# Kernel tuning notes

Measured on AMD Instinct MI355X. Metric: run time of the kernel, lower is better.

Reference implementation:

```python
import jax, jax.numpy as jnp
import numpy as np

DELTA_COEFF = 1.0
CLAMP_MIN = 1e-3  # hardcoded in original clamp(min=0.001)


def setup_inputs() -> dict:
    key = jax.random.key(0)
    k1, k2, k3 = jax.random.split(key, 3)
    B, N, F_in, F_out = 2, 1024, 128, 64
    x = jax.random.normal(k1, (B, N, F_in), dtype=jnp.float32)
    adj = jax.random.uniform(k2, (B, N, N), dtype=jnp.float32)
    weight = jax.random.normal(k3, (F_in, F_out), dtype=jnp.float32) * (1.0 / np.sqrt(F_in))
    bias = jnp.zeros((F_out,), dtype=jnp.float32)
    return {"x": x, "adj": adj, "weight": weight, "bias": bias}


def reference(x, adj, weight, bias):
    # x: [B,N,F_in], adj: [B,N,N]
    x = x @ weight  # [B,N,F_out]
    B, N, _ = adj.shape
    # pairwise L1 distance: [B,N,N]
    abs_diff = jnp.sum(jnp.abs(x[:, :, None, :] - x[:, None, :, :]), axis=-1)
    mod_adj = adj / jnp.maximum(abs_diff, CLAMP_MIN)
    deg = jnp.sum(mod_adj, axis=-1)  # [B,N]
    # Laplacian L = D - A~ ; then I - delta * L
    lap = jnp.zeros_like(mod_adj).at[:, jnp.arange(N), jnp.arange(N)].set(deg) - mod_adj
    mod = jnp.eye(N, dtype=x.dtype) - DELTA_COEFF * lap
    out = jnp.matmul(mod, x) + bias
    return out
```

## Files before the change

### kernel.cpp

```cpp
#include <hip/hip_runtime.h>
#include <hip/hip_fp16.h>


#define JS 16
#define HSTR 72

typedef _Float16 half8_t __attribute__((ext_vector_type(8)));
typedef float    f32x4_t __attribute__((ext_vector_type(4)));

__global__ __launch_bounds__(256) void gemm_xw(const float* __restrict__ x,
                                               const float* __restrict__ w,
                                               float* __restrict__ xw,
                                               __half* __restrict__ xwh,
                                               __half* __restrict__ xwt) {
    __shared__ float ws_[128 * 64];
    __shared__ float xs[8 * 132];
    __shared__ __half ts[8 * 64];
    const int tid = threadIdx.x;
    const int r0  = blockIdx.x * 8;

#pragma unroll
    for (int e = tid; e < 2048; e += 256)
        ((float4*)ws_)[e] = ((const float4*)w)[e];
    {
        int row = tid >> 5, c = tid & 31;
        float4 v = *(const float4*)&x[(size_t)(r0 + row) * 128 + c * 4];
        *(float4*)&xs[row * 132 + c * 4] = v;
    }
    __syncthreads();

    const int rl = tid >> 5;
    const int fg = tid & 31;
    float2 acc = {0.f, 0.f};
#pragma unroll 8
    for (int k = 0; k < 128; ++k) {
        float xv = xs[rl * 132 + k];
        float2 wv = *(const float2*)&ws_[k * 64 + 2 * fg];
        acc.x += xv * wv.x; acc.y += xv * wv.y;
    }
    size_t o = (size_t)(r0 + rl) * 64 + 2 * fg;
    *(float2*)&xw[o] = acc;
    __half2 h2 = __floats2half2_rn(acc.x, acc.y);
    *(__half2*)&xwh[o] = h2;
    *(__half2*)&ts[rl * 64 + 2 * fg] = h2;
    __syncthreads();

    if (tid < 64) {
        const int f = tid;
        const int b = r0 >> 10;
        const int n0 = r0 & 1023;
        __half hv[8];
#pragma unroll
        for (int r = 0; r < 8; ++r) hv[r] = ts[r * 64 + f];
        *(half8_t*)&xwt[((size_t)(b * 64 + f)) * 1024 + n0] = *(half8_t*)hv;
    }
}

template <bool ATOMIC>
__global__ __launch_bounds__(256) void fused_gtv(const __half* __restrict__ xwh,
                                                 const __half* __restrict__ xwt,
                                                 const float* __restrict__ adj,
                                                 float* __restrict__ pout,
                                                 float* __restrict__ pdeg) {
    __shared__ __half xih[32 * HSTR];
    __shared__ __half xjh[64 * HSTR];
    __shared__ __half xjt[64 * HSTR];
    __shared__ __half wt[32 * HSTR];

    const int tid = threadIdx.x;
    const int bx  = blockIdx.x;
    const int js  = bx & 15;
    const int it  = (bx >> 4) & 31;
    const int b   = bx >> 9;
    const int i0  = it * 32;
    const int j0  = js * 64;

    const __half* xhb = xwh + (size_t)b * 65536;
    const __half* xtb = xwt + (size_t)b * 65536;
    const float*  adjb = adj + (size_t)b * 1048576;

    const int ty = tid >> 5;
    const int tx = tid & 31;

    float2 av[4];
#pragma unroll
    for (int r = 0; r < 4; ++r)
        av[r] = *(const float2*)&adjb[(size_t)(i0 + 4 * ty + r) * 1024 + j0 + 2 * tx];

    {
        int row = tid >> 3, c = tid & 7;
        float4 v = *(const float4*)&xhb[(i0 + row) * 64 + c * 8];
        *(float4*)&xih[row * HSTR + c * 8] = v;
    }
#pragma unroll
    for (int e = tid; e < 512; e += 256) {
        int row = e >> 3, c = e & 7;
        float4 v = *(const float4*)&xhb[(j0 + row) * 64 + c * 8];
        *(float4*)&xjh[row * HSTR + c * 8] = v;
        float4 t = *(const float4*)&xtb[row * 1024 + j0 + c * 8];
        *(float4*)&xjt[row * HSTR + c * 8] = t;
    }
    __syncthreads();

    __half2 acc[4][2];
#pragma unroll
    for (int r = 0; r < 4; ++r)
#pragma unroll
        for (int q = 0; q < 2; ++q) acc[r][q] = __floats2half2_rn(0.f, 0.f);

#pragma unroll
    for (int c = 0; c < 8; ++c) {
        float4 a[4], bb[2];
#pragma unroll
        for (int r = 0; r < 4; ++r)
            a[r] = *(const float4*)&xih[(4 * ty + r) * HSTR + c * 8];
#pragma unroll
        for (int q = 0; q < 2; ++q)
            bb[q] = *(const float4*)&xjh[(2 * tx + q) * HSTR + c * 8];
#pragma unroll
        for (int r = 0; r < 4; ++r) {
            const __half2* pa = (const __half2*)&a[r];
#pragma unroll
            for (int q = 0; q < 2; ++q) {
                const __half2* pb = (const __half2*)&bb[q];
#pragma unroll
                for (int m = 0; m < 4; ++m)
                    acc[r][q] = __hadd2(acc[r][q], __habs2(__hsub2(pa[m], pb[m])));
            }
        }
    }

    float dsum[4];
#pragma unroll
    for (int r = 0; r < 4; ++r) {
        const int gi = i0 + 4 * ty + r;
        float wv[2];
#pragma unroll
        for (int q = 0; q < 2; ++q) {
            const int gj = j0 + 2 * tx + q;
            float d = __low2float(acc[r][q]) + __high2float(acc[r][q]);
            float v = (&av[r].x)[q] / fmaxf(d, 1e-3f);
            wv[q] = (gi == gj) ? 0.f : v;
        }
        *(__half2*)&wt[(4 * ty + r) * HSTR + 2 * tx] = __floats2half2_rn(wv[0], wv[1]);
        dsum[r] = wv[0] + wv[1];
    }
#pragma unroll
    for (int r = 0; r < 4; ++r) {
#pragma unroll
        for (int m = 1; m < 32; m <<= 1)
            dsum[r] += __shfl_xor(dsum[r], m, 32);
    }
    if (tx == 0) {
#pragma unroll
        for (int r = 0; r < 4; ++r) {
            if (ATOMIC) atomicAdd(&pdeg[b * 1024 + i0 + 4 * ty + r], dsum[r]);
            else pdeg[(js * 2 + b) * 1024 + i0 + 4 * ty + r] = dsum[r];
        }
    }
    __syncthreads();

    const int wv   = tid >> 6;
    const int lane = tid & 63;
    const int quad = lane >> 4;
    const int l15  = lane & 15;
    const int m16  = wv & 1;
    const int npair = wv >> 1;

    f32x4_t c0 = {0.f, 0.f, 0.f, 0.f};
    f32x4_t c1 = {0.f, 0.f, 0.f, 0.f};
#pragma unroll
    for (int s = 0; s < 2; ++s) {
        half8_t af = *(half8_t*)&wt[(m16 * 16 + l15) * HSTR + s * 32 + quad * 8];
        half8_t b0 = *(half8_t*)&xjt[((npair * 2 + 0) * 16 + l15) * HSTR + s * 32 + quad * 8];
        half8_t b1 = *(half8_t*)&xjt[((npair * 2 + 1) * 16 + l15) * HSTR + s * 32 + quad * 8];
        c0 = __builtin_amdgcn_mfma_f32_16x16x32_f16(af, b0, c0, 0, 0, 0);
        c1 = __builtin_amdgcn_mfma_f32_16x16x32_f16(af, b1, c1, 0, 0, 0);
    }

    if (ATOMIC) {
#pragma unroll
        for (int r = 0; r < 4; ++r) {
            int row = m16 * 16 + quad * 4 + r;
            atomicAdd(&pout[((size_t)b * 1024 + i0 + row) * 64 + (npair * 2) * 16 + l15], c0[r]);
            atomicAdd(&pout[((size_t)b * 1024 + i0 + row) * 64 + (npair * 2 + 1) * 16 + l15], c1[r]);
        }
    } else {
        const size_t slot = (size_t)(js * 2 + b) * 65536;
#pragma unroll
        for (int r = 0; r < 4; ++r) {
            int row = m16 * 16 + quad * 4 + r;
            pout[slot + (i0 + row) * 64 + (npair * 2) * 16 + l15] = c0[r];
            pout[slot + (i0 + row) * 64 + (npair * 2 + 1) * 16 + l15] = c1[r];
        }
    }
}

template <bool ATOMIC>
__global__ __launch_bounds__(256) void finish_gtv(const float* __restrict__ xw,
                                                  const float* __restrict__ part,
                                                  const float* __restrict__ pdeg,
                                                  const float* __restrict__ bias,
                                                  float* __restrict__ out) {
    int idx = blockIdx.x * 256 + threadIdx.x;
    int f = idx & 63;
    int r = idx >> 6;
    int b = r >> 10;
    if (ATOMIC) {
        out[idx] = out[idx] + (1.f - pdeg[r]) * xw[idx] + bias[f];
    } else {
        int loc = idx & 65535;
        int n   = r & 1023;
        float s = 0.f, dgs = 0.f;
#pragma unroll
        for (int js = 0; js < JS; ++js) {
            s   += part[(size_t)(js * 2 + b) * 65536 + loc];
            dgs += pdeg[(js * 2 + b) * 1024 + n];
        }
        out[idx] = s + (1.f - dgs) * xw[idx] + bias[f];
    }
}

extern "C" void kernel_launch(void* const* d_in, const int* in_sizes, int n_in,
                              void* d_out, int out_size, void* d_ws, size_t ws_size,
                              hipStream_t stream) {
    const float* x    = (const float*)d_in[0];
    const float* adj  = (const float*)d_in[1];
    const float* w    = (const float*)d_in[2];
    const float* bias = (const float*)d_in[3];
    float* out = (float*)d_out;

    char* wsb = (char*)d_ws;
    float*  xw   = (float*)wsb;
    __half* xwh  = (__half*)(wsb + 512 * 1024);
    __half* xwt  = (__half*)(wsb + 768 * 1024);
    float*  pdeg = (float*)(wsb + 1024 * 1024);
    float*  part = (float*)(wsb + 1152 * 1024);
    const size_t NEED = 1152 * 1024 + (size_t)32 * 65536 * 4;

    gemm_xw<<<256, 256, 0, stream>>>(x, w, xw, xwh, xwt);

    if (ws_size >= NEED) {
        fused_gtv<false><<<1024, 256, 0, stream>>>(xwh, xwt, adj, part, pdeg);
        finish_gtv<false><<<512, 256, 0, stream>>>(xw, part, pdeg, bias, out);
    } else {
        hipMemsetAsync(out, 0, 2 * 1024 * 64 * sizeof(float), stream);
        hipMemsetAsync(pdeg, 0, 2 * 1024 * sizeof(float), stream);
        fused_gtv<true><<<1024, 256, 0, stream>>>(xwh, xwt, adj, out, pdeg);
        finish_gtv<true><<<512, 256, 0, stream>>>(xw, nullptr, pdeg, bias, out);
    }
}
```

Before: 85.08 us.

## Enlarge fused tile to 64x64, swizzle LDS, store fp16 partials, vectorize xw GEMM

Each block of the fused kernel now covers a 64x64 i-j tile instead of 32x64, with a 4x4 per-thread micro-tile and four MFMA output tiles per wave. This halves the block count and increases reuse of the loaded features. LDS feature rows use an XOR swizzle to reduce bank conflicts. Partial output sums are stored as fp16 to halve workspace traffic in the finish kernel, which costs accuracy when the 16 partials are summed. The x@W GEMM loads x as float4 and fully unrolls the k loop.

```diff
diff --git a/kernel.cpp b/kernel.cpp
--- a/kernel.cpp
+++ b/kernel.cpp
@@ -5,6 +5,7 @@
 #define JS 16
 #define HSTR 72
 
+typedef _Float16 half4_t __attribute__((ext_vector_type(4)));
 typedef _Float16 half8_t __attribute__((ext_vector_type(8)));
 typedef float    f32x4_t __attribute__((ext_vector_type(4)));
 
@@ -32,11 +33,15 @@
     const int rl = tid >> 5;
     const int fg = tid & 31;
     float2 acc = {0.f, 0.f};
-#pragma unroll 8
-    for (int k = 0; k < 128; ++k) {
-        float xv = xs[rl * 132 + k];
-        float2 wv = *(const float2*)&ws_[k * 64 + 2 * fg];
-        acc.x += xv * wv.x; acc.y += xv * wv.y;
+#pragma unroll
+    for (int k4 = 0; k4 < 32; ++k4) {
+        float4 xv = *(const float4*)&xs[rl * 132 + k4 * 4];
+        const float* xp = &xv.x;
+#pragma unroll
+        for (int m = 0; m < 4; ++m) {
+            float2 wv = *(const float2*)&ws_[(k4 * 4 + m) * 64 + 2 * fg];
+            acc.x += xp[m] * wv.x; acc.y += xp[m] * wv.y;
+        }
     }
     size_t o = (size_t)(r0 + rl) * 64 + 2 * fg;
     *(float2*)&xw[o] = acc;
@@ -60,68 +65,69 @@
 __global__ __launch_bounds__(256) void fused_gtv(const __half* __restrict__ xwh,
                                                  const __half* __restrict__ xwt,
                                                  const float* __restrict__ adj,
-                                                 float* __restrict__ pout,
+                                                 __half* __restrict__ part,
+                                                 float* __restrict__ aout,
                                                  float* __restrict__ pdeg) {
-    __shared__ __half xih[32 * HSTR];
+    __shared__ __half xih[64 * HSTR];
     __shared__ __half xjh[64 * HSTR];
     __shared__ __half xjt[64 * HSTR];
-    __shared__ __half wt[32 * HSTR];
+    __shared__ __half wt [64 * HSTR];
 
     const int tid = threadIdx.x;
     const int bx  = blockIdx.x;
     const int js  = bx & 15;
-    const int it  = (bx >> 4) & 31;
-    const int b   = bx >> 9;
-    const int i0  = it * 32;
+    const int it  = (bx >> 4) & 15;
+    const int b   = bx >> 8;
+    const int i0  = it * 64;
     const int j0  = js * 64;
 
     const __half* xhb = xwh + (size_t)b * 65536;
     const __half* xtb = xwt + (size_t)b * 65536;
     const float*  adjb = adj + (size_t)b * 1048576;
 
-    const int ty = tid >> 5;
-    const int tx = tid & 31;
-
-    float2 av[4];
+    const int ty = tid >> 4;
+    const int tx = tid & 15;
+
+    float4 av[4];
 #pragma unroll
     for (int r = 0; r < 4; ++r)
-        av[r] = *(const float2*)&adjb[(size_t)(i0 + 4 * ty + r) * 1024 + j0 + 2 * tx];
-
-    {
-        int row = tid >> 3, c = tid & 7;
-        float4 v = *(const float4*)&xhb[(i0 + row) * 64 + c * 8];
-        *(float4*)&xih[row * HSTR + c * 8] = v;
-    }
+        av[r] = *(const float4*)&adjb[(size_t)(i0 + 4 * ty + r) * 1024 + j0 + 4 * tx];
+
 #pragma unroll
     for (int e = tid; e < 512; e += 256) {
-        int row = e >> 3, c = e & 7;
-        float4 v = *(const float4*)&xhb[(j0 + row) * 64 + c * 8];
-        *(float4*)&xjh[row * HSTR + c * 8] = v;
-        float4 t = *(const float4*)&xtb[row * 1024 + j0 + c * 8];
-        *(float4*)&xjt[row * HSTR + c * 8] = t;
-    }
-    __syncthreads();
-
-    __half2 acc[4][2];
+        int row = e >> 3, cb = e & 7;
+        int sc = ((cb ^ ((row >> 2) & 7)) << 3);
+        float4 vi = *(const float4*)&xhb[(i0 + row) * 64 + cb * 8];
+        *(float4*)&xih[row * HSTR + sc] = vi;
+        float4 vj = *(const float4*)&xhb[(j0 + row) * 64 + cb * 8];
+        *(float4*)&xjh[row * HSTR + sc] = vj;
+        float4 vt = *(const float4*)&xtb[row * 1024 + j0 + cb * 8];
+        *(float4*)&xjt[row * HSTR + cb * 8] = vt;
+    }
+    __syncthreads();
+
+    __half2 acc[4][4];
 #pragma unroll
     for (int r = 0; r < 4; ++r)
 #pragma unroll
-        for (int q = 0; q < 2; ++q) acc[r][q] = __floats2half2_rn(0.f, 0.f);
+        for (int q = 0; q < 4; ++q) acc[r][q] = __floats2half2_rn(0.f, 0.f);
 
 #pragma unroll
     for (int c = 0; c < 8; ++c) {
-        float4 a[4], bb[2];
+        const int ca = ((c ^ (ty & 7)) << 3);
+        const int cb = ((c ^ (tx & 7)) << 3);
+        float4 a[4], bb[4];
 #pragma unroll
         for (int r = 0; r < 4; ++r)
-            a[r] = *(const float4*)&xih[(4 * ty + r) * HSTR + c * 8];
-#pragma unroll
-        for (int q = 0; q < 2; ++q)
-            bb[q] = *(const float4*)&xjh[(2 * tx + q) * HSTR + c * 8];
+            a[r] = *(const float4*)&xih[(4 * ty + r) * HSTR + ca];
+#pragma unroll
+        for (int q = 0; q < 4; ++q)
+            bb[q] = *(const float4*)&xjh[(4 * tx + q) * HSTR + cb];
 #pragma unroll
         for (int r = 0; r < 4; ++r) {
             const __half2* pa = (const __half2*)&a[r];
 #pragma unroll
-            for (int q = 0; q < 2; ++q) {
+            for (int q = 0; q < 4; ++q) {
                 const __half2* pb = (const __half2*)&bb[q];
 #pragma unroll
                 for (int m = 0; m < 4; ++m)
@@ -134,22 +140,25 @@
 #pragma unroll
     for (int r = 0; r < 4; ++r) {
         const int gi = i0 + 4 * ty + r;
-        float wv[2];
-#pragma unroll
-        for (int q = 0; q < 2; ++q) {
-            const int gj = j0 + 2 * tx + q;
+        float wv[4];
+        dsum[r] = 0.f;
+#pragma unroll
+        for (int q = 0; q < 4; ++q) {
             float d = __low2float(acc[r][q]) + __high2float(acc[r][q]);
             float v = (&av[r].x)[q] / fmaxf(d, 1e-3f);
-            wv[q] = (gi == gj) ? 0.f : v;
-        }
-        *(__half2*)&wt[(4 * ty + r) * HSTR + 2 * tx] = __floats2half2_rn(wv[0], wv[1]);
-        dsum[r] = wv[0] + wv[1];
+            wv[q] = (gi == j0 + 4 * tx + q) ? 0.f : v;
+            dsum[r] += wv[q];
+        }
+        float2 packed;
+        ((__half2*)&packed)[0] = __floats2half2_rn(wv[0], wv[1]);
+        ((__half2*)&packed)[1] = __floats2half2_rn(wv[2], wv[3]);
+        *(float2*)&wt[(4 * ty + r) * HSTR + 4 * tx] = packed;
     }
 #pragma unroll
     for (int r = 0; r < 4; ++r) {
 #pragma unroll
-        for (int m = 1; m < 32; m <<= 1)
-            dsum[r] += __shfl_xor(dsum[r], m, 32);
+        for (int m = 1; m < 16; m <<= 1)
+            dsum[r] += __shfl_xor(dsum[r], m, 16);
     }
     if (tx == 0) {
 #pragma unroll
@@ -160,45 +169,45 @@
     }
     __syncthreads();
 
-    const int wv   = tid >> 6;
+    const int wv_  = tid >> 6;
     const int lane = tid & 63;
     const int quad = lane >> 4;
     const int l15  = lane & 15;
-    const int m16  = wv & 1;
-    const int npair = wv >> 1;
-
-    f32x4_t c0 = {0.f, 0.f, 0.f, 0.f};
-    f32x4_t c1 = {0.f, 0.f, 0.f, 0.f};
-#pragma unroll
-    for (int s = 0; s < 2; ++s) {
-        half8_t af = *(half8_t*)&wt[(m16 * 16 + l15) * HSTR + s * 32 + quad * 8];
-        half8_t b0 = *(half8_t*)&xjt[((npair * 2 + 0) * 16 + l15) * HSTR + s * 32 + quad * 8];
-        half8_t b1 = *(half8_t*)&xjt[((npair * 2 + 1) * 16 + l15) * HSTR + s * 32 + quad * 8];
-        c0 = __builtin_amdgcn_mfma_f32_16x16x32_f16(af, b0, c0, 0, 0, 0);
-        c1 = __builtin_amdgcn_mfma_f32_16x16x32_f16(af, b1, c1, 0, 0, 0);
+
+    f32x4_t c[4] = {{0,0,0,0},{0,0,0,0},{0,0,0,0},{0,0,0,0}};
+    half8_t a0 = *(half8_t*)&wt[(wv_ * 16 + l15) * HSTR + quad * 8];
+    half8_t a1 = *(half8_t*)&wt[(wv_ * 16 + l15) * HSTR + 32 + quad * 8];
+#pragma unroll
+    for (int n = 0; n < 4; ++n) {
+        half8_t b0 = *(half8_t*)&xjt[(n * 16 + l15) * HSTR + quad * 8];
+        half8_t b1 = *(half8_t*)&xjt[(n * 16 + l15) * HSTR + 32 + quad * 8];
+        c[n] = __builtin_amdgcn_mfma_f32_16x16x32_f16(a0, b0, c[n], 0, 0, 0);
+        c[n] = __builtin_amdgcn_mfma_f32_16x16x32_f16(a1, b1, c[n], 0, 0, 0);
     }
 
     if (ATOMIC) {
 #pragma unroll
-        for (int r = 0; r < 4; ++r) {
-            int row = m16 * 16 + quad * 4 + r;
-            atomicAdd(&pout[((size_t)b * 1024 + i0 + row) * 64 + (npair * 2) * 16 + l15], c0[r]);
-            atomicAdd(&pout[((size_t)b * 1024 + i0 + row) * 64 + (npair * 2 + 1) * 16 + l15], c1[r]);
-        }
+        for (int n = 0; n < 4; ++n)
+#pragma unroll
+            for (int r = 0; r < 4; ++r) {
+                int row = wv_ * 16 + quad * 4 + r;
+                atomicAdd(&aout[((size_t)b * 1024 + i0 + row) * 64 + n * 16 + l15], c[n][r]);
+            }
     } else {
         const size_t slot = (size_t)(js * 2 + b) * 65536;
 #pragma unroll
-        for (int r = 0; r < 4; ++r) {
-            int row = m16 * 16 + quad * 4 + r;
-            pout[slot + (i0 + row) * 64 + (npair * 2) * 16 + l15] = c0[r];
-            pout[slot + (i0 + row) * 64 + (npair * 2 + 1) * 16 + l15] = c1[r];
-        }
+        for (int n = 0; n < 4; ++n)
+#pragma unroll
+            for (int r = 0; r < 4; ++r) {
+                int row = wv_ * 16 + quad * 4 + r;
+                part[slot + (i0 + row) * 64 + n * 16 + l15] = __float2half(c[n][r]);
+            }
     }
 }
 
 template <bool ATOMIC>
 __global__ __launch_bounds__(256) void finish_gtv(const float* __restrict__ xw,
-                                                  const float* __restrict__ part,
+                                                  const __half* __restrict__ part,
                                                   const float* __restrict__ pdeg,
                                                   const float* __restrict__ bias,
                                                   float* __restrict__ out) {
@@ -214,7 +223,7 @@
         float s = 0.f, dgs = 0.f;
 #pragma unroll
         for (int js = 0; js < JS; ++js) {
-            s   += part[(size_t)(js * 2 + b) * 65536 + loc];
+            s   += __half2float(part[(size_t)(js * 2 + b) * 65536 + loc]);
             dgs += pdeg[(js * 2 + b) * 1024 + n];
         }
         out[idx] = s + (1.f - dgs) * xw[idx] + bias[f];
@@ -235,18 +244,18 @@
     __half* xwh  = (__half*)(wsb + 512 * 1024);
     __half* xwt  = (__half*)(wsb + 768 * 1024);
     float*  pdeg = (float*)(wsb + 1024 * 1024);
-    float*  part = (float*)(wsb + 1152 * 1024);
-    const size_t NEED = 1152 * 1024 + (size_t)32 * 65536 * 4;
+    __half* part = (__half*)(wsb + 1152 * 1024);
+    const size_t NEED = 1152 * 1024 + (size_t)32 * 65536 * 2;
 
     gemm_xw<<<256, 256, 0, stream>>>(x, w, xw, xwh, xwt);
 
     if (ws_size >= NEED) {
-        fused_gtv<false><<<1024, 256, 0, stream>>>(xwh, xwt, adj, part, pdeg);
+        fused_gtv<false><<<512, 256, 0, stream>>>(xwh, xwt, adj, part, nullptr, pdeg);
         finish_gtv<false><<<512, 256, 0, stream>>>(xw, part, pdeg, bias, out);
     } else {
         hipMemsetAsync(out, 0, 2 * 1024 * 64 * sizeof(float), stream);
         hipMemsetAsync(pdeg, 0, 2 * 1024 * sizeof(float), stream);
-        fused_gtv<true><<<1024, 256, 0, stream>>>(xwh, xwt, adj, out, pdeg);
+        fused_gtv<true><<<512, 256, 0, stream>>>(xwh, xwt, adj, nullptr, out, pdeg);
         finish_gtv<true><<<512, 256, 0, stream>>>(xw, nullptr, pdeg, bias, out);
     }
 }
```

Measured after the change: 84.15 us. About the same (-1.1%).
